# Kernel optimization log

Hardware: AMD Instinct MI355X
Metric: run time of the kernel (lower is better)

## Reference

```python
import jax, jax.numpy as jnp
import numpy as np

CH = 512
HEADS = 8
REDUCTION = 2
INNER = max(CH // REDUCTION, HEADS)  # 256
POS_RES = 16
LN_EPS = 1e-5


def setup_inputs() -> dict:
    key = jax.random.key(0)
    ks = jax.random.split(key, 7)
    B, H, W = 1, 64, 64
    x = jax.random.normal(ks[0], (B, CH, H, W), dtype=jnp.float32)
    w_qkv = jax.random.normal(ks[1], (INNER * 3, CH), dtype=jnp.float32) * 0.02
    w_proj = jax.random.normal(ks[2], (CH, INNER), dtype=jnp.float32) * 0.02
    b_proj = jnp.zeros((CH,), dtype=jnp.float32)
    pos_bias = jax.random.normal(ks[3], (1, HEADS, POS_RES, POS_RES), dtype=jnp.float32) * 0.02
    gamma = jnp.ones((CH,), dtype=jnp.float32)
    beta = jnp.zeros((CH,), dtype=jnp.float32)
    return {"x": x, "w_qkv": w_qkv, "w_proj": w_proj, "b_proj": b_proj,
            "pos_bias": pos_bias, "gamma": gamma, "beta": beta}


def reference(x, w_qkv, w_proj, b_proj, pos_bias, gamma, beta):
    B, C, H, W = x.shape
    d_head = INNER // HEADS
    scale = jnp.float32(d_head ** -0.5)

    # 1x1 conv == channel matmul
    qkv = jnp.einsum('oc,bchw->bohw', w_qkv, x)  # [B, 3*inner, H, W]
    q, k, v = jnp.split(qkv, 3, axis=1)

    def heads_view(t):
        return t.reshape(B, HEADS, d_head, H * W)  # [B, h, d, HW]

    q, k, v = heads_view(q), heads_view(k), heads_view(v)

    attn = jnp.einsum('bhdi,bhdj->bhij', q * scale, k)  # [B, h, HW, HW]

    # bilinear interp of pos bias 16x16 -> HxW (half-pixel, matches align_corners=False)
    pos = jax.image.resize(pos_bias, (1, HEADS, H, W), method='bilinear')
    pos = pos.reshape(1, HEADS, H * W)
    attn = attn + pos[..., :, None] + pos[..., None, :]

    attn = jax.nn.softmax(attn, axis=-1)
    y = jnp.einsum('bhij,bhdj->bhdi', attn, v)  # [B, h, d, HW]
    y = y.reshape(B, INNER, H, W)

    y = jnp.einsum('co,bohw->bchw', w_proj, y) + b_proj[None, :, None, None]

    # LayerNorm over channel dim of (x + y)
    z = (x + y).transpose(0, 2, 3, 1)  # [B, H, W, C]
    mu = jnp.mean(z, axis=-1, keepdims=True)
    var = jnp.var(z, axis=-1, keepdims=True)
    z = (z - mu) / jnp.sqrt(var + LN_EPS) * gamma + beta
    return z.transpose(0, 3, 1, 2)
```

## Files before the change

### kernel.cpp

```cpp
#include <hip/hip_runtime.h>
#include <hip/hip_bf16.h>
#include <math.h>

#define HW 4096
#define LN_EPS 1e-5f

typedef _Float16 half4v __attribute__((ext_vector_type(4)));
typedef _Float16 half8v __attribute__((ext_vector_type(8)));
typedef float float4v __attribute__((ext_vector_type(4)));
typedef __fp16 fp16v2 __attribute__((ext_vector_type(2)));
typedef __fp16 fp16v4 __attribute__((ext_vector_type(4)));

#if __has_builtin(__builtin_amdgcn_exp2f)
#define EXP2F(x) __builtin_amdgcn_exp2f(x)
#else
#define EXP2F(x) exp2f(x)
#endif

__device__ __forceinline__ half4v lo4(half8v v) { return __builtin_shufflevector(v, v, 0, 1, 2, 3); }
__device__ __forceinline__ half4v hi4(half8v v) { return __builtin_shufflevector(v, v, 4, 5, 6, 7); }

__device__ __forceinline__ void gload_lds16(const _Float16* g, _Float16* l) {
#if __has_builtin(__builtin_amdgcn_global_load_lds)
    __builtin_amdgcn_global_load_lds(
        (const __attribute__((address_space(1))) void*)(const void*)g,
        (__attribute__((address_space(3))) void*)(void*)l, 16, 0, 0);
#else
    int lane = threadIdx.x & 63;
    *(half8v*)(l + lane * 8) = *(const half8v*)g;
#endif
}

__global__ __launch_bounds__(256) void k_pre(const float* __restrict__ x,
                                             const float* __restrict__ wq,
                                             const float* __restrict__ wp,
                                             const float* __restrict__ pb,
                                             _Float16* __restrict__ xt,
                                             _Float16* __restrict__ wqh,
                                             _Float16* __restrict__ wph,
                                             float* __restrict__ pos) {
    int bx = blockIdx.x, t = threadIdx.x;
    if (bx < 512) {
        __shared__ _Float16 tile[64][65];
        int c0 = (bx >> 6) * 64, p0 = (bx & 63) * 64;
        int w = t >> 6, lane = t & 63;
        #pragma unroll
        for (int r = 0; r < 16; r++)
            tile[w * 16 + r][lane] = (_Float16)x[(c0 + w * 16 + r) * HW + p0 + lane];
        __syncthreads();
        int cg = (t & 15) * 4, pr = t >> 4;
        #pragma unroll
        for (int r = 0; r < 4; r++) {
            int p = pr + r * 16;
            half4v v;
            #pragma unroll
            for (int k = 0; k < 4; k++) v[k] = tile[cg + k][p];
            *(half4v*)&xt[(p0 + p) * 512 + c0 + cg] = v;
        }
        return;
    }
    int i = (bx - 512) * 256 + t;
    const float qs = 0.17677669529663687f * 1.4426950408889634f;
    if (i < 49152) {
        float s = (i < 16384) ? qs : 1.0f;
        float4v a = *(const float4v*)(wq + i * 8);
        float4v b = *(const float4v*)(wq + i * 8 + 4);
        half8v h;
        #pragma unroll
        for (int k = 0; k < 4; k++) { h[k] = (_Float16)(a[k] * s); h[4 + k] = (_Float16)(b[k] * s); }
        *(half8v*)(wqh + i * 8) = h;
    } else if (i < 65536) {
        int j = i - 49152;
        float4v a = *(const float4v*)(wp + j * 8);
        float4v b = *(const float4v*)(wp + j * 8 + 4);
        half8v h;
        #pragma unroll
        for (int k = 0; k < 4; k++) { h[k] = (_Float16)a[k]; h[4 + k] = (_Float16)b[k]; }
        *(half8v*)(wph + j * 8) = h;
    } else {
        int j = i - 65536;
        int h = j >> 12, p = j & 4095, y = p >> 6, xx = p & 63;
        float sy = y * 0.25f - 0.375f, sx = xx * 0.25f - 0.375f;
        float fy = floorf(sy), fx = floorf(sx);
        float wy = sy - fy, wx = sx - fx;
        int y0 = (int)fy, x0 = (int)fx;
        int y1 = y0 + 1 < 15 ? y0 + 1 : 15;
        int x1 = x0 + 1 < 15 ? x0 + 1 : 15;
        y0 = y0 > 0 ? y0 : 0;
        x0 = x0 > 0 ? x0 : 0;
        const float* src = pb + h * 256;
        float v = (1.f - wy) * ((1.f - wx) * src[y0 * 16 + x0] + wx * src[y0 * 16 + x1]) +
                  wy * ((1.f - wx) * src[y1 * 16 + x0] + wx * src[y1 * 16 + x1]);
        pos[j] = v * 1.4426950408889634f;
    }
}

__global__ __launch_bounds__(256) void k_qkv(const _Float16* __restrict__ wqh,
                                             const _Float16* __restrict__ xt,
                                             _Float16* __restrict__ qa,
                                             _Float16* __restrict__ ka,
                                             _Float16* __restrict__ va) {
    int n0 = (blockIdx.x >> 5) * 64;
    int p0 = (blockIdx.x & 31) * 128;
    int t = threadIdx.x, w = t >> 6, lane = t & 63, quad = lane >> 4, l16 = lane & 15;

    const _Float16* aptr0 = xt + (p0 + w * 16 + l16) * 512 + quad * 8;
    const _Float16* aptr1 = aptr0 + 64 * 512;
    const _Float16* bptr = wqh + (n0 + l16) * 512 + quad * 8;

    float4v acc[2][4] = {};
    #pragma unroll 4
    for (int kc = 0; kc < 16; kc++) {
        half8v a0 = *(const half8v*)(aptr0 + kc * 32);
        half8v a1 = *(const half8v*)(aptr1 + kc * 32);
        #pragma unroll
        for (int nt = 0; nt < 4; nt++) {
            half8v b = *(const half8v*)(bptr + nt * 16 * 512 + kc * 32);
            acc[0][nt] = __builtin_amdgcn_mfma_f32_16x16x32_f16(a0, b, acc[0][nt], 0, 0, 0);
            acc[1][nt] = __builtin_amdgcn_mfma_f32_16x16x32_f16(a1, b, acc[1][nt], 0, 0, 0);
        }
    }
    #pragma unroll
    for (int ps = 0; ps < 2; ps++) {
        #pragma unroll
        for (int nt = 0; nt < 4; nt++) {
            int o = n0 + nt * 16 + l16;
            #pragma unroll
            for (int r = 0; r < 4; r++) {
                int p = p0 + ps * 64 + w * 16 + quad * 4 + r;
                _Float16 v = (_Float16)acc[ps][nt][r];
                if (o < 256) {
                    qa[(o >> 5) * 131072 + p * 32 + (o & 31)] = v;
                } else if (o < 512) {
                    int oc = o - 256, hh = oc >> 5, d = oc & 31;
                    ka[hh * 131072 + (p >> 4) * 512 + ((d >> 3) * 16 + (p & 15)) * 8 + (d & 7)] = v;
                } else {
                    int oc = o - 512, hh = oc >> 5, d = oc & 31;
                    va[hh * 131072 + (p >> 4) * 512 + (((p >> 2) & 3) * 16 + (d & 15)) * 8 +
                       (d >> 4) * 4 + (p & 3)] = v;
                }
            }
        }
    }
}

__global__ __launch_bounds__(256, 4) void k_attn(const _Float16* __restrict__ qa,
                                                 const _Float16* __restrict__ ka,
                                                 const _Float16* __restrict__ va,
                                                 const float* __restrict__ pos,
                                                 float* __restrict__ op,
                                                 float* __restrict__ lp) {
    __shared__ __attribute__((aligned(16))) _Float16 kbuf[2][2048];
    __shared__ __attribute__((aligned(16))) _Float16 vbuf[2][2048];
    __shared__ __attribute__((aligned(16))) float posl[1024];
    int h = blockIdx.x & 7;
    int jq = (blockIdx.x >> 3) & 3;
    int qb = blockIdx.x >> 5;
    int t = threadIdx.x, w = t >> 6, lane = t & 63, quad = lane >> 4, l16 = lane & 15;
    int q0 = qb * 128 + w * 32;

    float* opp = op + jq * 1048576;
    float* lpp = lp + jq * 32768;

    *(float4v*)(posl + t * 4) = *(const float4v*)(pos + h * HW + jq * 1024 + t * 4);

    half8v qf0 = *(const half8v*)(qa + h * 131072 + (q0 + l16) * 32 + quad * 8);
    half8v qf1 = *(const half8v*)(qa + h * 131072 + (q0 + 16 + l16) * 32 + quad * 8);

    const _Float16* kg = ka + h * 131072 + jq * 32768;
    const _Float16* vg = va + h * 131072 + jq * 32768;

    gload_lds16(kg + (w * 64 + lane) * 8, &kbuf[0][w * 512]);
    gload_lds16(vg + (w * 64 + lane) * 8, &vbuf[0][w * 512]);

    float4v o00 = {}, o01 = {}, o10 = {}, o11 = {};
    float lsum0 = 0.f, lsum1 = 0.f;
    const fp16v2 one2 = {(__fp16)1.0f, (__fp16)1.0f};

    for (int tile = 0; tile < 16; tile++) {
        int buf = tile & 1;
        __syncthreads();
        if (tile + 1 < 16) {
            gload_lds16(kg + (tile + 1) * 2048 + (w * 64 + lane) * 8, &kbuf[buf ^ 1][w * 512]);
            gload_lds16(vg + (tile + 1) * 2048 + (w * 64 + lane) * 8, &vbuf[buf ^ 1][w * 512]);
        }
        #pragma unroll
        for (int w16 = 0; w16 < 4; w16++) {
            half8v kf = *(const half8v*)(kbuf[buf] + w16 * 512 + lane * 8);
            half8v vf = *(const half8v*)(vbuf[buf] + w16 * 512 + lane * 8);
            float4v pbv = *(const float4v*)(posl + tile * 64 + w16 * 16 + quad * 4);

            float4v s0 = __builtin_amdgcn_mfma_f32_16x16x32_f16(kf, qf0, pbv, 0, 0, 0);
            float4v s1 = __builtin_amdgcn_mfma_f32_16x16x32_f16(kf, qf1, pbv, 0, 0, 0);

            float e0 = EXP2F(s0[0]);
            float e1 = EXP2F(s0[1]);
            float e2 = EXP2F(s0[2]);
            float e3 = EXP2F(s0[3]);
            float f0 = EXP2F(s1[0]);
            float f1 = EXP2F(s1[1]);
            float f2 = EXP2F(s1[2]);
            float f3 = EXP2F(s1[3]);

            fp16v2 a01 = __builtin_amdgcn_cvt_pkrtz(e0, e1);
            fp16v2 a23 = __builtin_amdgcn_cvt_pkrtz(e2, e3);
            fp16v2 b01 = __builtin_amdgcn_cvt_pkrtz(f0, f1);
            fp16v2 b23 = __builtin_amdgcn_cvt_pkrtz(f2, f3);
            half4v pa0 = __builtin_bit_cast(half4v, __builtin_shufflevector(a01, a23, 0, 1, 2, 3));
            half4v pa1 = __builtin_bit_cast(half4v, __builtin_shufflevector(b01, b23, 0, 1, 2, 3));

#if __has_builtin(__builtin_amdgcn_fdot2)
            lsum0 = __builtin_amdgcn_fdot2(a01, one2, lsum0, false);
            lsum0 = __builtin_amdgcn_fdot2(a23, one2, lsum0, false);
            lsum1 = __builtin_amdgcn_fdot2(b01, one2, lsum1, false);
            lsum1 = __builtin_amdgcn_fdot2(b23, one2, lsum1, false);
#else
            lsum0 += (e0 + e1) + (e2 + e3);
            lsum1 += (f0 + f1) + (f2 + f3);
#endif
            o00 = __builtin_amdgcn_mfma_f32_16x16x16f16(pa0, lo4(vf), o00, 0, 0, 0);
            o01 = __builtin_amdgcn_mfma_f32_16x16x16f16(pa0, hi4(vf), o01, 0, 0, 0);
            o10 = __builtin_amdgcn_mfma_f32_16x16x16f16(pa1, lo4(vf), o10, 0, 0, 0);
            o11 = __builtin_amdgcn_mfma_f32_16x16x16f16(pa1, hi4(vf), o11, 0, 0, 0);
        }
    }
    lsum0 += __shfl_xor(lsum0, 16, 64);
    lsum0 += __shfl_xor(lsum0, 32, 64);
    lsum1 += __shfl_xor(lsum1, 16, 64);
    lsum1 += __shfl_xor(lsum1, 32, 64);
    #pragma unroll
    for (int r = 0; r < 4; r++) {
        int qr = quad * 4 + r;
        int qi0 = q0 + qr, qi1 = q0 + 16 + qr;
        opp[qi0 * 256 + h * 32 + l16] = o00[r];
        opp[qi0 * 256 + h * 32 + 16 + l16] = o01[r];
        opp[qi1 * 256 + h * 32 + l16] = o10[r];
        opp[qi1 * 256 + h * 32 + 16 + l16] = o11[r];
    }
    if (quad == 0) {
        lpp[(q0 + l16) * 8 + h] = lsum0;
        lpp[(q0 + 16 + l16) * 8 + h] = lsum1;
    }
}

__global__ __launch_bounds__(1024) void k_proj_ln(const _Float16* __restrict__ wph,
                                                  const float* __restrict__ op,
                                                  const float* __restrict__ lp,
                                                  const float* __restrict__ x,
                                                  const float* __restrict__ b_proj,
                                                  const float* __restrict__ gamma,
                                                  const float* __restrict__ beta,
                                                  float* __restrict__ out) {
    __shared__ __attribute__((aligned(16))) _Float16 ys[16 * 264];
    __shared__ float red[2][16][17];
    int p0 = blockIdx.x * 16;
    int t = threadIdx.x, w = t >> 6, lane = t & 63, quad = lane >> 4, l16 = lane & 15;
    {
        int p = t >> 6, cg = (t & 63) * 4;
        int pi = p0 + p;
        float4v a0 = *(const float4v*)(op + pi * 256 + cg);
        float4v a1 = *(const float4v*)(op + 1048576 + pi * 256 + cg);
        float4v a2 = *(const float4v*)(op + 2097152 + pi * 256 + cg);
        float4v a3 = *(const float4v*)(op + 3145728 + pi * 256 + cg);
        int hh = cg >> 5;
        float l = lp[pi * 8 + hh] + lp[32768 + pi * 8 + hh] +
                  lp[65536 + pi * 8 + hh] + lp[98304 + pi * 8 + hh];
        float inv = 1.f / l;
        half4v y;
        #pragma unroll
        for (int k = 0; k < 4; k++) y[k] = (_Float16)(((a0[k] + a1[k]) + (a2[k] + a3[k])) * inv);
        *(half4v*)(ys + p * 264 + cg) = y;
    }
    __syncthreads();
    float4v acc[2] = {};
    #pragma unroll
    for (int kc = 0; kc < 8; kc++) {
        half8v b = *(const half8v*)(ys + l16 * 264 + kc * 32 + quad * 8);
        #pragma unroll
        for (int mt = 0; mt < 2; mt++) {
            half8v a = *(const half8v*)(wph + (w * 32 + mt * 16 + l16) * 256 + kc * 32 + quad * 8);
            acc[mt] = __builtin_amdgcn_mfma_f32_16x16x32_f16(a, b, acc[mt], 0, 0, 0);
        }
    }
    int p = p0 + l16;
    float sum = 0.f, sumsq = 0.f;
    #pragma unroll
    for (int mt = 0; mt < 2; mt++)
        #pragma unroll
        for (int r = 0; r < 4; r++) {
            int c = w * 32 + mt * 16 + quad * 4 + r;
            float v = acc[mt][r] + b_proj[c] + x[c * HW + p];
            acc[mt][r] = v;
            sum += v;
            sumsq += v * v;
        }
    sum += __shfl_xor(sum, 16, 64);
    sum += __shfl_xor(sum, 32, 64);
    sumsq += __shfl_xor(sumsq, 16, 64);
    sumsq += __shfl_xor(sumsq, 32, 64);
    if (quad == 0) { red[0][w][l16] = sum; red[1][w][l16] = sumsq; }
    __syncthreads();
    float s0 = 0.f, s1 = 0.f;
    #pragma unroll
    for (int ww = 0; ww < 16; ww++) { s0 += red[0][ww][l16]; s1 += red[1][ww][l16]; }
    float mean = s0 * (1.f / 512.f);
    float var = s1 * (1.f / 512.f) - mean * mean;
    float rstd = rsqrtf(var + LN_EPS);
    #pragma unroll
    for (int mt = 0; mt < 2; mt++)
        #pragma unroll
        for (int r = 0; r < 4; r++) {
            int c = w * 32 + mt * 16 + quad * 4 + r;
            out[c * HW + p] = (acc[mt][r] - mean) * rstd * gamma[c] + beta[c];
        }
}

extern "C" void kernel_launch(void* const* d_in, const int* in_sizes, int n_in,
                              void* d_out, int out_size, void* d_ws, size_t ws_size,
                              hipStream_t stream) {
    const float* x      = (const float*)d_in[0];
    const float* w_qkv  = (const float*)d_in[1];
    const float* w_proj = (const float*)d_in[2];
    const float* b_proj = (const float*)d_in[3];
    const float* pos_b  = (const float*)d_in[4];
    const float* gamma  = (const float*)d_in[5];
    const float* beta   = (const float*)d_in[6];
    char* ws = (char*)d_ws;
    _Float16* xt  = (_Float16*)(ws);
    _Float16* qa  = (_Float16*)(ws + 4194304);
    _Float16* ka  = (_Float16*)(ws + 6291456);
    _Float16* va  = (_Float16*)(ws + 8388608);
    float*    op  = (float*)   (ws + 10485760);
    float*    lp  = (float*)   (ws + 27262976);
    float*    pos = (float*)   (ws + 27787264);
    _Float16* wqh = (_Float16*)(ws + 27918336);
    _Float16* wph = (_Float16*)(ws + 28704768);

    k_pre<<<896, 256, 0, stream>>>(x, w_qkv, w_proj, pos_b, xt, wqh, wph, pos);
    k_qkv<<<384, 256, 0, stream>>>(wqh, xt, qa, ka, va);
    k_attn<<<1024, 256, 0, stream>>>(qa, ka, va, pos, op, lp);
    k_proj_ln<<<256, 1024, 0, stream>>>(wph, op, lp, x, b_proj, gamma, beta, (float*)d_out);
}
```

Before: 139.9 us.

## Fuse four stages into one cooperative persistent kernel with grid syncs

Merges the preprocessing, QKV projection, attention and projection+LayerNorm stages into a single cooperative kernel that separates phases with grid-wide barriers. The goal is to remove the overhead and tail gaps of four separate kernel launches. To keep one 256-thread block shape across all phases, the QKV GEMM tile is halved and the proj/LN phase moves from 1024 to 256 threads, each wave covering 128 channels. This costs more per-thread register pressure in the LN phase, grid-sync overhead, and possible occupancy limits on the fused kernel. Separate kernels remain as a fallback if the cooperative launch fails.

```diff
diff --git a/kernel.cpp b/kernel.cpp
--- a/kernel.cpp
+++ b/kernel.cpp
@@ -1,15 +1,17 @@
 #include <hip/hip_runtime.h>
 #include <hip/hip_bf16.h>
+#include <hip/hip_cooperative_groups.h>
 #include <math.h>
 
 #define HW 4096
 #define LN_EPS 1e-5f
+
+namespace cg = cooperative_groups;
 
 typedef _Float16 half4v __attribute__((ext_vector_type(4)));
 typedef _Float16 half8v __attribute__((ext_vector_type(8)));
 typedef float float4v __attribute__((ext_vector_type(4)));
 typedef __fp16 fp16v2 __attribute__((ext_vector_type(2)));
-typedef __fp16 fp16v4 __attribute__((ext_vector_type(4)));
 
 #if __has_builtin(__builtin_amdgcn_exp2f)
 #define EXP2F(x) __builtin_amdgcn_exp2f(x)
@@ -31,52 +33,52 @@
 #endif
 }
 
-__global__ __launch_bounds__(256) void k_pre(const float* __restrict__ x,
-                                             const float* __restrict__ wq,
-                                             const float* __restrict__ wp,
-                                             const float* __restrict__ pb,
-                                             _Float16* __restrict__ xt,
-                                             _Float16* __restrict__ wqh,
-                                             _Float16* __restrict__ wph,
-                                             float* __restrict__ pos) {
-    int bx = blockIdx.x, t = threadIdx.x;
-    if (bx < 512) {
-        __shared__ _Float16 tile[64][65];
-        int c0 = (bx >> 6) * 64, p0 = (bx & 63) * 64;
-        int w = t >> 6, lane = t & 63;
+struct P {
+    const float *x, *wq, *wp, *b_proj, *pb, *gamma, *beta;
+    _Float16 *xt, *qa, *ka, *va;
+    float *op, *lp, *pos;
+    _Float16 *wqh, *wph;
+    float* out;
+};
+
+__device__ __forceinline__ void phaseA(int u, int t, char* smem, const P& pp) {
+    int w = t >> 6, lane = t & 63;
+    if (u < 512) {
+        _Float16 (*tile)[65] = (_Float16(*)[65])smem;
+        int c0 = (u >> 6) * 64, p0 = (u & 63) * 64;
         #pragma unroll
         for (int r = 0; r < 16; r++)
-            tile[w * 16 + r][lane] = (_Float16)x[(c0 + w * 16 + r) * HW + p0 + lane];
+            tile[w * 16 + r][lane] = (_Float16)pp.x[(c0 + w * 16 + r) * HW + p0 + lane];
         __syncthreads();
-        int cg = (t & 15) * 4, pr = t >> 4;
+        int cgx = (t & 15) * 4, pr = t >> 4;
         #pragma unroll
         for (int r = 0; r < 4; r++) {
             int p = pr + r * 16;
             half4v v;
             #pragma unroll
-            for (int k = 0; k < 4; k++) v[k] = tile[cg + k][p];
-            *(half4v*)&xt[(p0 + p) * 512 + c0 + cg] = v;
+            for (int k = 0; k < 4; k++) v[k] = tile[cgx + k][p];
+            *(half4v*)&pp.xt[(p0 + p) * 512 + c0 + cgx] = v;
         }
         return;
     }
-    int i = (bx - 512) * 256 + t;
+    int i = (u - 512) * 256 + t;
     const float qs = 0.17677669529663687f * 1.4426950408889634f;
     if (i < 49152) {
         float s = (i < 16384) ? qs : 1.0f;
-        float4v a = *(const float4v*)(wq + i * 8);
-        float4v b = *(const float4v*)(wq + i * 8 + 4);
+        float4v a = *(const float4v*)(pp.wq + i * 8);
+        float4v b = *(const float4v*)(pp.wq + i * 8 + 4);
         half8v h;
         #pragma unroll
         for (int k = 0; k < 4; k++) { h[k] = (_Float16)(a[k] * s); h[4 + k] = (_Float16)(b[k] * s); }
-        *(half8v*)(wqh + i * 8) = h;
+        *(half8v*)(pp.wqh + i * 8) = h;
     } else if (i < 65536) {
         int j = i - 49152;
-        float4v a = *(const float4v*)(wp + j * 8);
-        float4v b = *(const float4v*)(wp + j * 8 + 4);
+        float4v a = *(const float4v*)(pp.wp + j * 8);
+        float4v b = *(const float4v*)(pp.wp + j * 8 + 4);
         half8v h;
         #pragma unroll
         for (int k = 0; k < 4; k++) { h[k] = (_Float16)a[k]; h[4 + k] = (_Float16)b[k]; }
-        *(half8v*)(wph + j * 8) = h;
+        *(half8v*)(pp.wph + j * 8) = h;
     } else {
         int j = i - 65536;
         int h = j >> 12, p = j & 4095, y = p >> 6, xx = p & 63;
@@ -88,90 +90,72 @@
         int x1 = x0 + 1 < 15 ? x0 + 1 : 15;
         y0 = y0 > 0 ? y0 : 0;
         x0 = x0 > 0 ? x0 : 0;
-        const float* src = pb + h * 256;
+        const float* src = pp.pb + h * 256;
         float v = (1.f - wy) * ((1.f - wx) * src[y0 * 16 + x0] + wx * src[y0 * 16 + x1]) +
                   wy * ((1.f - wx) * src[y1 * 16 + x0] + wx * src[y1 * 16 + x1]);
-        pos[j] = v * 1.4426950408889634f;
-    }
-}
-
-__global__ __launch_bounds__(256) void k_qkv(const _Float16* __restrict__ wqh,
-                                             const _Float16* __restrict__ xt,
-                                             _Float16* __restrict__ qa,
-                                             _Float16* __restrict__ ka,
-                                             _Float16* __restrict__ va) {
-    int n0 = (blockIdx.x >> 5) * 64;
-    int p0 = (blockIdx.x & 31) * 128;
-    int t = threadIdx.x, w = t >> 6, lane = t & 63, quad = lane >> 4, l16 = lane & 15;
-
-    const _Float16* aptr0 = xt + (p0 + w * 16 + l16) * 512 + quad * 8;
-    const _Float16* aptr1 = aptr0 + 64 * 512;
-    const _Float16* bptr = wqh + (n0 + l16) * 512 + quad * 8;
-
-    float4v acc[2][4] = {};
+        pp.pos[j] = v * 1.4426950408889634f;
+    }
+}
+
+__device__ __forceinline__ void phaseB(int u, int t, const P& pp) {
+    int w = t >> 6, lane = t & 63, quad = lane >> 4, l16 = lane & 15;
+    int n0 = (u >> 6) * 64;
+    int p0 = (u & 63) * 64;
+    const _Float16* aptr = pp.xt + (p0 + w * 16 + l16) * 512 + quad * 8;
+    const _Float16* bptr = pp.wqh + (n0 + l16) * 512 + quad * 8;
+    float4v acc[4] = {};
     #pragma unroll 4
     for (int kc = 0; kc < 16; kc++) {
-        half8v a0 = *(const half8v*)(aptr0 + kc * 32);
-        half8v a1 = *(const half8v*)(aptr1 + kc * 32);
+        half8v a = *(const half8v*)(aptr + kc * 32);
         #pragma unroll
         for (int nt = 0; nt < 4; nt++) {
             half8v b = *(const half8v*)(bptr + nt * 16 * 512 + kc * 32);
-            acc[0][nt] = __builtin_amdgcn_mfma_f32_16x16x32_f16(a0, b, acc[0][nt], 0, 0, 0);
-            acc[1][nt] = __builtin_amdgcn_mfma_f32_16x16x32_f16(a1, b, acc[1][nt], 0, 0, 0);
-        }
-    }
-    #pragma unroll
-    for (int ps = 0; ps < 2; ps++) {
-        #pragma unroll
-        for (int nt = 0; nt < 4; nt++) {
-            int o = n0 + nt * 16 + l16;
-            #pragma unroll
-            for (int r = 0; r < 4; r++) {
-                int p = p0 + ps * 64 + w * 16 + quad * 4 + r;
-                _Float16 v = (_Float16)acc[ps][nt][r];
-                if (o < 256) {
-                    qa[(o >> 5) * 131072 + p * 32 + (o & 31)] = v;
-                } else if (o < 512) {
-                    int oc = o - 256, hh = oc >> 5, d = oc & 31;
-                    ka[hh * 131072 + (p >> 4) * 512 + ((d >> 3) * 16 + (p & 15)) * 8 + (d & 7)] = v;
-                } else {
-                    int oc = o - 512, hh = oc >> 5, d = oc & 31;
-                    va[hh * 131072 + (p >> 4) * 512 + (((p >> 2) & 3) * 16 + (d & 15)) * 8 +
-                       (d >> 4) * 4 + (p & 3)] = v;
-                }
+            acc[nt] = __builtin_amdgcn_mfma_f32_16x16x32_f16(a, b, acc[nt], 0, 0, 0);
+        }
+    }
+    #pragma unroll
+    for (int nt = 0; nt < 4; nt++) {
+        int o = n0 + nt * 16 + l16;
+        #pragma unroll
+        for (int r = 0; r < 4; r++) {
+            int p = p0 + w * 16 + quad * 4 + r;
+            _Float16 v = (_Float16)acc[nt][r];
+            if (o < 256) {
+                pp.qa[(o >> 5) * 131072 + p * 32 + (o & 31)] = v;
+            } else if (o < 512) {
+                int oc = o - 256, hh = oc >> 5, d = oc & 31;
+                pp.ka[hh * 131072 + (p >> 4) * 512 + ((d >> 3) * 16 + (p & 15)) * 8 + (d & 7)] = v;
+            } else {
+                int oc = o - 512, hh = oc >> 5, d = oc & 31;
+                pp.va[hh * 131072 + (p >> 4) * 512 + (((p >> 2) & 3) * 16 + (d & 15)) * 8 +
+                      (d >> 4) * 4 + (p & 3)] = v;
             }
         }
     }
 }
 
-__global__ __launch_bounds__(256, 4) void k_attn(const _Float16* __restrict__ qa,
-                                                 const _Float16* __restrict__ ka,
-                                                 const _Float16* __restrict__ va,
-                                                 const float* __restrict__ pos,
-                                                 float* __restrict__ op,
-                                                 float* __restrict__ lp) {
-    __shared__ __attribute__((aligned(16))) _Float16 kbuf[2][2048];
-    __shared__ __attribute__((aligned(16))) _Float16 vbuf[2][2048];
-    __shared__ __attribute__((aligned(16))) float posl[1024];
-    int h = blockIdx.x & 7;
-    int jq = (blockIdx.x >> 3) & 3;
-    int qb = blockIdx.x >> 5;
-    int t = threadIdx.x, w = t >> 6, lane = t & 63, quad = lane >> 4, l16 = lane & 15;
+__device__ __forceinline__ void phaseC(int u, int t, char* smem, const P& pp) {
+    _Float16* kbuf = (_Float16*)smem;
+    _Float16* vbuf = (_Float16*)(smem + 8192);
+    float* posl = (float*)(smem + 16384);
+    int w = t >> 6, lane = t & 63, quad = lane >> 4, l16 = lane & 15;
+    int h = u & 7;
+    int jq = (u >> 3) & 3;
+    int qb = u >> 5;
     int q0 = qb * 128 + w * 32;
-
-    float* opp = op + jq * 1048576;
-    float* lpp = lp + jq * 32768;
-
-    *(float4v*)(posl + t * 4) = *(const float4v*)(pos + h * HW + jq * 1024 + t * 4);
-
-    half8v qf0 = *(const half8v*)(qa + h * 131072 + (q0 + l16) * 32 + quad * 8);
-    half8v qf1 = *(const half8v*)(qa + h * 131072 + (q0 + 16 + l16) * 32 + quad * 8);
-
-    const _Float16* kg = ka + h * 131072 + jq * 32768;
-    const _Float16* vg = va + h * 131072 + jq * 32768;
-
-    gload_lds16(kg + (w * 64 + lane) * 8, &kbuf[0][w * 512]);
-    gload_lds16(vg + (w * 64 + lane) * 8, &vbuf[0][w * 512]);
+    float* opp = pp.op + jq * 1048576;
+    float* lpp = pp.lp + jq * 32768;
+
+    *(float4v*)(posl + t * 4) = *(const float4v*)(pp.pos + h * HW + jq * 1024 + t * 4);
+
+    half8v qf0 = *(const half8v*)(pp.qa + h * 131072 + (q0 + l16) * 32 + quad * 8);
+    half8v qf1 = *(const half8v*)(pp.qa + h * 131072 + (q0 + 16 + l16) * 32 + quad * 8);
+
+    const _Float16* kg = pp.ka + h * 131072 + jq * 32768;
+    const _Float16* vg = pp.va + h * 131072 + jq * 32768;
+
+    gload_lds16(kg + (w * 64 + lane) * 8, kbuf + w * 512);
+    gload_lds16(vg + (w * 64 + lane) * 8, vbuf + w * 512);
 
     float4v o00 = {}, o01 = {}, o10 = {}, o11 = {};
     float lsum0 = 0.f, lsum1 = 0.f;
@@ -181,13 +165,15 @@
         int buf = tile & 1;
         __syncthreads();
         if (tile + 1 < 16) {
-            gload_lds16(kg + (tile + 1) * 2048 + (w * 64 + lane) * 8, &kbuf[buf ^ 1][w * 512]);
-            gload_lds16(vg + (tile + 1) * 2048 + (w * 64 + lane) * 8, &vbuf[buf ^ 1][w * 512]);
+            gload_lds16(kg + (tile + 1) * 2048 + (w * 64 + lane) * 8,
+                        kbuf + (buf ^ 1) * 2048 + w * 512);
+            gload_lds16(vg + (tile + 1) * 2048 + (w * 64 + lane) * 8,
+                        vbuf + (buf ^ 1) * 2048 + w * 512);
         }
         #pragma unroll
         for (int w16 = 0; w16 < 4; w16++) {
-            half8v kf = *(const half8v*)(kbuf[buf] + w16 * 512 + lane * 8);
-            half8v vf = *(const half8v*)(vbuf[buf] + w16 * 512 + lane * 8);
+            half8v kf = *(const half8v*)(kbuf + buf * 2048 + w16 * 512 + lane * 8);
+            half8v vf = *(const half8v*)(vbuf + buf * 2048 + w16 * 512 + lane * 8);
             float4v pbv = *(const float4v*)(posl + tile * 64 + w16 * 16 + quad * 4);
 
             float4v s0 = __builtin_amdgcn_mfma_f32_16x16x32_f16(kf, qf0, pbv, 0, 0, 0);
@@ -243,53 +229,48 @@
     }
 }
 
-__global__ __launch_bounds__(1024) void k_proj_ln(const _Float16* __restrict__ wph,
-                                                  const float* __restrict__ op,
-                                                  const float* __restrict__ lp,
-                                                  const float* __restrict__ x,
-                                                  const float* __restrict__ b_proj,
-                                                  const float* __restrict__ gamma,
-                                                  const float* __restrict__ beta,
-                                                  float* __restrict__ out) {
-    __shared__ __attribute__((aligned(16))) _Float16 ys[16 * 264];
-    __shared__ float red[2][16][17];
-    int p0 = blockIdx.x * 16;
-    int t = threadIdx.x, w = t >> 6, lane = t & 63, quad = lane >> 4, l16 = lane & 15;
-    {
-        int p = t >> 6, cg = (t & 63) * 4;
+__device__ __forceinline__ void phaseD(int u, int t, char* smem, const P& pp) {
+    _Float16* ys = (_Float16*)smem;
+    float (*red)[4][16] = (float(*)[4][16])(smem + 8448);
+    int w = t >> 6, lane = t & 63, quad = lane >> 4, l16 = lane & 15;
+    int p0 = u * 16;
+    #pragma unroll
+    for (int g4 = 0; g4 < 4; g4++) {
+        int g = t + g4 * 256;
+        int p = g >> 6, cgx = (g & 63) * 4;
         int pi = p0 + p;
-        float4v a0 = *(const float4v*)(op + pi * 256 + cg);
-        float4v a1 = *(const float4v*)(op + 1048576 + pi * 256 + cg);
-        float4v a2 = *(const float4v*)(op + 2097152 + pi * 256 + cg);
-        float4v a3 = *(const float4v*)(op + 3145728 + pi * 256 + cg);
-        int hh = cg >> 5;
-        float l = lp[pi * 8 + hh] + lp[32768 + pi * 8 + hh] +
-                  lp[65536 + pi * 8 + hh] + lp[98304 + pi * 8 + hh];
+        float4v a0 = *(const float4v*)(pp.op + pi * 256 + cgx);
+        float4v a1 = *(const float4v*)(pp.op + 1048576 + pi * 256 + cgx);
+        float4v a2 = *(const float4v*)(pp.op + 2097152 + pi * 256 + cgx);
+        float4v a3 = *(const float4v*)(pp.op + 3145728 + pi * 256 + cgx);
+        int hh = cgx >> 5;
+        float l = pp.lp[pi * 8 + hh] + pp.lp[32768 + pi * 8 + hh] +
+                  pp.lp[65536 + pi * 8 + hh] + pp.lp[98304 + pi * 8 + hh];
         float inv = 1.f / l;
-        half4v y;
-        #pragma unroll
-        for (int k = 0; k < 4; k++) y[k] = (_Float16)(((a0[k] + a1[k]) + (a2[k] + a3[k])) * inv);
-        *(half4v*)(ys + p * 264 + cg) = y;
+        half4v yv;
+        #pragma unroll
+        for (int k = 0; k < 4; k++) yv[k] = (_Float16)(((a0[k] + a1[k]) + (a2[k] + a3[k])) * inv);
+        *(half4v*)(ys + p * 264 + cgx) = yv;
     }
     __syncthreads();
-    float4v acc[2] = {};
+    float4v acc[8] = {};
     #pragma unroll
     for (int kc = 0; kc < 8; kc++) {
         half8v b = *(const half8v*)(ys + l16 * 264 + kc * 32 + quad * 8);
         #pragma unroll
-        for (int mt = 0; mt < 2; mt++) {
-            half8v a = *(const half8v*)(wph + (w * 32 + mt * 16 + l16) * 256 + kc * 32 + quad * 8);
+        for (int mt = 0; mt < 8; mt++) {
+            half8v a = *(const half8v*)(pp.wph + (w * 128 + mt * 16 + l16) * 256 + kc * 32 + quad * 8);
             acc[mt] = __builtin_amdgcn_mfma_f32_16x16x32_f16(a, b, acc[mt], 0, 0, 0);
         }
     }
     int p = p0 + l16;
     float sum = 0.f, sumsq = 0.f;
     #pragma unroll
-    for (int mt = 0; mt < 2; mt++)
+    for (int mt = 0; mt < 8; mt++)
         #pragma unroll
         for (int r = 0; r < 4; r++) {
-            int c = w * 32 + mt * 16 + quad * 4 + r;
-            float v = acc[mt][r] + b_proj[c] + x[c * HW + p];
+            int c = w * 128 + mt * 16 + quad * 4 + r;
+            float v = acc[mt][r] + pp.b_proj[c] + pp.x[c * HW + p];
             acc[mt][r] = v;
             sum += v;
             sumsq += v * v;
@@ -300,44 +281,88 @@
     sumsq += __shfl_xor(sumsq, 32, 64);
     if (quad == 0) { red[0][w][l16] = sum; red[1][w][l16] = sumsq; }
     __syncthreads();
-    float s0 = 0.f, s1 = 0.f;
-    #pragma unroll
-    for (int ww = 0; ww < 16; ww++) { s0 += red[0][ww][l16]; s1 += red[1][ww][l16]; }
+    float s0 = (red[0][0][l16] + red[0][1][l16]) + (red[0][2][l16] + red[0][3][l16]);
+    float s1 = (red[1][0][l16] + red[1][1][l16]) + (red[1][2][l16] + red[1][3][l16]);
     float mean = s0 * (1.f / 512.f);
     float var = s1 * (1.f / 512.f) - mean * mean;
     float rstd = rsqrtf(var + LN_EPS);
     #pragma unroll
-    for (int mt = 0; mt < 2; mt++)
+    for (int mt = 0; mt < 8; mt++)
         #pragma unroll
         for (int r = 0; r < 4; r++) {
-            int c = w * 32 + mt * 16 + quad * 4 + r;
-            out[c * HW + p] = (acc[mt][r] - mean) * rstd * gamma[c] + beta[c];
-        }
+            int c = w * 128 + mt * 16 + quad * 4 + r;
+            pp.out[c * HW + p] = (acc[mt][r] - mean) * rstd * pp.gamma[c] + pp.beta[c];
+        }
+}
+
+__global__ __launch_bounds__(256, 4) void k_coop(P pp) {
+    __shared__ __attribute__((aligned(16))) char smem[24576];
+    cg::grid_group grid = cg::this_grid();
+    int G = gridDim.x, bid = blockIdx.x, t = threadIdx.x;
+    for (int u = bid; u < 896; u += G) { __syncthreads(); phaseA(u, t, smem, pp); }
+    __threadfence();
+    grid.sync();
+    for (int u = bid; u < 768; u += G) phaseB(u, t, pp);
+    __threadfence();
+    grid.sync();
+    for (int u = bid; u < 1024; u += G) { __syncthreads(); phaseC(u, t, smem, pp); }
+    __threadfence();
+    grid.sync();
+    for (int u = bid; u < 256; u += G) { __syncthreads(); phaseD(u, t, smem, pp); }
+}
+
+__global__ __launch_bounds__(256) void kA(P pp) {
+    __shared__ __attribute__((aligned(16))) char smem[8320];
+    phaseA(blockIdx.x, threadIdx.x, smem, pp);
+}
+__global__ __launch_bounds__(256) void kB(P pp) { phaseB(blockIdx.x, threadIdx.x, pp); }
+__global__ __launch_bounds__(256, 4) void kC(P pp) {
+    __shared__ __attribute__((aligned(16))) char smem[24576];
+    phaseC(blockIdx.x, threadIdx.x, smem, pp);
+}
+__global__ __launch_bounds__(256) void kD(P pp) {
+    __shared__ __attribute__((aligned(16))) char smem[9216];
+    phaseD(blockIdx.x, threadIdx.x, smem, pp);
 }
 
 extern "C" void kernel_launch(void* const* d_in, const int* in_sizes, int n_in,
                               void* d_out, int out_size, void* d_ws, size_t ws_size,
                               hipStream_t stream) {
-    const float* x      = (const float*)d_in[0];
-    const float* w_qkv  = (const float*)d_in[1];
-    const float* w_proj = (const float*)d_in[2];
-    const float* b_proj = (const float*)d_in[3];
-    const float* pos_b  = (const float*)d_in[4];
-    const float* gamma  = (const float*)d_in[5];
-    const float* beta   = (const float*)d_in[6];
     char* ws = (char*)d_ws;
-    _Float16* xt  = (_Float16*)(ws);
-    _Float16* qa  = (_Float16*)(ws + 4194304);
-    _Float16* ka  = (_Float16*)(ws + 6291456);
-    _Float16* va  = (_Float16*)(ws + 8388608);
-    float*    op  = (float*)   (ws + 10485760);
-    float*    lp  = (float*)   (ws + 27262976);
-    float*    pos = (float*)   (ws + 27787264);
-    _Float16* wqh = (_Float16*)(ws + 27918336);
-    _Float16* wph = (_Float16*)(ws + 28704768);
-
-    k_pre<<<896, 256, 0, stream>>>(x, w_qkv, w_proj, pos_b, xt, wqh, wph, pos);
-    k_qkv<<<384, 256, 0, stream>>>(wqh, xt, qa, ka, va);
-    k_attn<<<1024, 256, 0, stream>>>(qa, ka, va, pos, op, lp);
-    k_proj_ln<<<256, 1024, 0, stream>>>(wph, op, lp, x, b_proj, gamma, beta, (float*)d_out);
-}
+    P pp;
+    pp.x      = (const float*)d_in[0];
+    pp.wq     = (const float*)d_in[1];
+    pp.wp     = (const float*)d_in[2];
+    pp.b_proj = (const float*)d_in[3];
+    pp.pb     = (const float*)d_in[4];
+    pp.gamma  = (const float*)d_in[5];
+    pp.beta   = (const float*)d_in[6];
+    pp.xt  = (_Float16*)(ws);
+    pp.qa  = (_Float16*)(ws + 4194304);
+    pp.ka  = (_Float16*)(ws + 6291456);
+    pp.va  = (_Float16*)(ws + 8388608);
+    pp.op  = (float*)   (ws + 10485760);
+    pp.lp  = (float*)   (ws + 27262976);
+    pp.pos = (float*)   (ws + 27787264);
+    pp.wqh = (_Float16*)(ws + 27918336);
+    pp.wph = (_Float16*)(ws + 28704768);
+    pp.out = (float*)d_out;
+
+    int occ = 0;
+    hipError_t e = hipOccupancyMaxActiveBlocksPerMultiprocessor(&occ, (const void*)k_coop, 256, 0);
+    bool done = false;
+    if (e == hipSuccess && occ > 0) {
+        int grid = occ * 256;
+        if (grid > 1024) grid = 1024;
+        void* args[] = {&pp};
+        if (hipLaunchCooperativeKernel((void*)k_coop, dim3(grid), dim3(256), args, 0, stream)
+            == hipSuccess)
+            done = true;
+    }
+    if (!done) {
+        kA<<<896, 256, 0, stream>>>(pp);
+        kB<<<768, 256, 0, stream>>>(pp);
+        kC<<<1024, 256, 0, stream>>>(pp);
+        kD<<<256, 256, 0, stream>>>(pp);
+    }
+}
```

Result: slower. 537.1 us (+284.0%).

## Fuse preprocessing into QKV and attention kernels, drop pre-pass launch

Applied to the files above, without the earlier changes.

Removes the separate k_pre kernel. The QKV GEMM now reads fp32 x directly, transposes and converts it through an LDS tile, and converts and scales w_qkv on the fly. The proj-weight conversion moves into the first 128 QKV blocks, and the bilinear pos-bias interpolation is computed per attention block in shared memory. This saves a launch and the xt/pos intermediate round-trips through HBM, at the cost of redundant weight conversion across blocks, strided uncoalesced-ish fp32 loads of x, and extra per-block setup work in attention.

```diff
diff --git a/kernel.cpp b/kernel.cpp
--- a/kernel.cpp
+++ b/kernel.cpp
@@ -9,7 +9,6 @@
 typedef _Float16 half8v __attribute__((ext_vector_type(8)));
 typedef float float4v __attribute__((ext_vector_type(4)));
 typedef __fp16 fp16v2 __attribute__((ext_vector_type(2)));
-typedef __fp16 fp16v4 __attribute__((ext_vector_type(4)));
 
 #if __has_builtin(__builtin_amdgcn_exp2f)
 #define EXP2F(x) __builtin_amdgcn_exp2f(x)
@@ -31,93 +30,63 @@
 #endif
 }
 
-__global__ __launch_bounds__(256) void k_pre(const float* __restrict__ x,
+__global__ __launch_bounds__(256) void k_qkv(const float* __restrict__ x,
                                              const float* __restrict__ wq,
                                              const float* __restrict__ wp,
-                                             const float* __restrict__ pb,
-                                             _Float16* __restrict__ xt,
-                                             _Float16* __restrict__ wqh,
                                              _Float16* __restrict__ wph,
-                                             float* __restrict__ pos) {
-    int bx = blockIdx.x, t = threadIdx.x;
-    if (bx < 512) {
-        __shared__ _Float16 tile[64][65];
-        int c0 = (bx >> 6) * 64, p0 = (bx & 63) * 64;
-        int w = t >> 6, lane = t & 63;
-        #pragma unroll
-        for (int r = 0; r < 16; r++)
-            tile[w * 16 + r][lane] = (_Float16)x[(c0 + w * 16 + r) * HW + p0 + lane];
-        __syncthreads();
-        int cg = (t & 15) * 4, pr = t >> 4;
-        #pragma unroll
-        for (int r = 0; r < 4; r++) {
-            int p = pr + r * 16;
-            half4v v;
-            #pragma unroll
-            for (int k = 0; k < 4; k++) v[k] = tile[cg + k][p];
-            *(half4v*)&xt[(p0 + p) * 512 + c0 + cg] = v;
-        }
-        return;
-    }
-    int i = (bx - 512) * 256 + t;
-    const float qs = 0.17677669529663687f * 1.4426950408889634f;
-    if (i < 49152) {
-        float s = (i < 16384) ? qs : 1.0f;
-        float4v a = *(const float4v*)(wq + i * 8);
-        float4v b = *(const float4v*)(wq + i * 8 + 4);
-        half8v h;
-        #pragma unroll
-        for (int k = 0; k < 4; k++) { h[k] = (_Float16)(a[k] * s); h[4 + k] = (_Float16)(b[k] * s); }
-        *(half8v*)(wqh + i * 8) = h;
-    } else if (i < 65536) {
-        int j = i - 49152;
-        float4v a = *(const float4v*)(wp + j * 8);
-        float4v b = *(const float4v*)(wp + j * 8 + 4);
-        half8v h;
-        #pragma unroll
-        for (int k = 0; k < 4; k++) { h[k] = (_Float16)a[k]; h[4 + k] = (_Float16)b[k]; }
-        *(half8v*)(wph + j * 8) = h;
-    } else {
-        int j = i - 65536;
-        int h = j >> 12, p = j & 4095, y = p >> 6, xx = p & 63;
-        float sy = y * 0.25f - 0.375f, sx = xx * 0.25f - 0.375f;
-        float fy = floorf(sy), fx = floorf(sx);
-        float wy = sy - fy, wx = sx - fx;
-        int y0 = (int)fy, x0 = (int)fx;
-        int y1 = y0 + 1 < 15 ? y0 + 1 : 15;
-        int x1 = x0 + 1 < 15 ? x0 + 1 : 15;
-        y0 = y0 > 0 ? y0 : 0;
-        x0 = x0 > 0 ? x0 : 0;
-        const float* src = pb + h * 256;
-        float v = (1.f - wy) * ((1.f - wx) * src[y0 * 16 + x0] + wx * src[y0 * 16 + x1]) +
-                  wy * ((1.f - wx) * src[y1 * 16 + x0] + wx * src[y1 * 16 + x1]);
-        pos[j] = v * 1.4426950408889634f;
-    }
-}
-
-__global__ __launch_bounds__(256) void k_qkv(const _Float16* __restrict__ wqh,
-                                             const _Float16* __restrict__ xt,
                                              _Float16* __restrict__ qa,
                                              _Float16* __restrict__ ka,
                                              _Float16* __restrict__ va) {
-    int n0 = (blockIdx.x >> 5) * 64;
-    int p0 = (blockIdx.x & 31) * 128;
-    int t = threadIdx.x, w = t >> 6, lane = t & 63, quad = lane >> 4, l16 = lane & 15;
-
-    const _Float16* aptr0 = xt + (p0 + w * 16 + l16) * 512 + quad * 8;
-    const _Float16* aptr1 = aptr0 + 64 * 512;
-    const _Float16* bptr = wqh + (n0 + l16) * 512 + quad * 8;
+    __shared__ __attribute__((aligned(16))) _Float16 xs[128][72];
+    int bid = blockIdx.x, t = threadIdx.x;
+    int w = t >> 6, lane = t & 63, quad = lane >> 4, l16 = lane & 15;
+    const float qs = 0.17677669529663687f * 1.4426950408889634f;
+
+    if (bid < 128) {
+        int i = bid * 1024 + t * 4;
+        float4v a = *(const float4v*)(wp + i);
+        half4v h;
+        #pragma unroll
+        for (int k = 0; k < 4; k++) h[k] = (_Float16)a[k];
+        *(half4v*)(wph + i) = h;
+    }
+
+    int n0 = (bid >> 5) * 64;
+    int p0 = (bid & 31) * 128;
+    int sp = t & 127;
+    int sg = (t >> 7) * 32;
 
     float4v acc[2][4] = {};
-    #pragma unroll 4
-    for (int kc = 0; kc < 16; kc++) {
-        half8v a0 = *(const half8v*)(aptr0 + kc * 32);
-        half8v a1 = *(const half8v*)(aptr1 + kc * 32);
-        #pragma unroll
-        for (int nt = 0; nt < 4; nt++) {
-            half8v b = *(const half8v*)(bptr + nt * 16 * 512 + kc * 32);
-            acc[0][nt] = __builtin_amdgcn_mfma_f32_16x16x32_f16(a0, b, acc[0][nt], 0, 0, 0);
-            acc[1][nt] = __builtin_amdgcn_mfma_f32_16x16x32_f16(a1, b, acc[1][nt], 0, 0, 0);
+    for (int k0 = 0; k0 < 512; k0 += 64) {
+        __syncthreads();
+        #pragma unroll
+        for (int cc8 = 0; cc8 < 4; cc8++) {
+            int cb = sg + cc8 * 8;
+            half8v v;
+            #pragma unroll
+            for (int c = 0; c < 8; c++) v[c] = (_Float16)x[(k0 + cb + c) * HW + p0 + sp];
+            *(half8v*)&xs[sp][cb] = v;
+        }
+        __syncthreads();
+        #pragma unroll
+        for (int kc2 = 0; kc2 < 2; kc2++) {
+            half8v a0 = *(const half8v*)&xs[w * 16 + l16][kc2 * 32 + quad * 8];
+            half8v a1 = *(const half8v*)&xs[64 + w * 16 + l16][kc2 * 32 + quad * 8];
+            #pragma unroll
+            for (int nt = 0; nt < 4; nt++) {
+                float s = (n0 + nt * 16 < 256) ? qs : 1.0f;
+                const float* wr = wq + (n0 + nt * 16 + l16) * 512 + k0 + kc2 * 32 + quad * 8;
+                float4v b0 = *(const float4v*)wr;
+                float4v b1 = *(const float4v*)(wr + 4);
+                half8v b;
+                #pragma unroll
+                for (int k = 0; k < 4; k++) {
+                    b[k] = (_Float16)(b0[k] * s);
+                    b[4 + k] = (_Float16)(b1[k] * s);
+                }
+                acc[0][nt] = __builtin_amdgcn_mfma_f32_16x16x32_f16(a0, b, acc[0][nt], 0, 0, 0);
+                acc[1][nt] = __builtin_amdgcn_mfma_f32_16x16x32_f16(a1, b, acc[1][nt], 0, 0, 0);
+            }
         }
     }
     #pragma unroll
@@ -147,31 +116,49 @@
 __global__ __launch_bounds__(256, 4) void k_attn(const _Float16* __restrict__ qa,
                                                  const _Float16* __restrict__ ka,
                                                  const _Float16* __restrict__ va,
-                                                 const float* __restrict__ pos,
+                                                 const float* __restrict__ pb,
                                                  float* __restrict__ op,
                                                  float* __restrict__ lp) {
-    __shared__ __attribute__((aligned(16))) _Float16 kbuf[2][2048];
-    __shared__ __attribute__((aligned(16))) _Float16 vbuf[2][2048];
-    __shared__ __attribute__((aligned(16))) float posl[1024];
+    __shared__ __attribute__((aligned(16))) char smem[21504];
+    _Float16* kbuf = (_Float16*)smem;
+    _Float16* vbuf = (_Float16*)(smem + 8192);
+    float* posl = (float*)(smem + 16384);
+    float* pbl = (float*)(smem + 20480);
     int h = blockIdx.x & 7;
     int jq = (blockIdx.x >> 3) & 3;
     int qb = blockIdx.x >> 5;
     int t = threadIdx.x, w = t >> 6, lane = t & 63, quad = lane >> 4, l16 = lane & 15;
     int q0 = qb * 128 + w * 32;
-
     float* opp = op + jq * 1048576;
     float* lpp = lp + jq * 32768;
 
-    *(float4v*)(posl + t * 4) = *(const float4v*)(pos + h * HW + jq * 1024 + t * 4);
+    const _Float16* kg = ka + h * 131072 + jq * 32768;
+    const _Float16* vg = va + h * 131072 + jq * 32768;
+
+    gload_lds16(kg + (w * 64 + lane) * 8, kbuf + w * 512);
+    gload_lds16(vg + (w * 64 + lane) * 8, vbuf + w * 512);
+
+    pbl[t] = pb[h * 256 + t];
+    __syncthreads();
+    #pragma unroll
+    for (int k = 0; k < 4; k++) {
+        int j = jq * 1024 + t * 4 + k;
+        int y = j >> 6, xx = j & 63;
+        float sy = y * 0.25f - 0.375f, sx = xx * 0.25f - 0.375f;
+        float fy = floorf(sy), fx = floorf(sx);
+        float wy = sy - fy, wx = sx - fx;
+        int y0 = (int)fy, x0 = (int)fx;
+        int y1 = y0 + 1 < 15 ? y0 + 1 : 15;
+        int x1 = x0 + 1 < 15 ? x0 + 1 : 15;
+        y0 = y0 > 0 ? y0 : 0;
+        x0 = x0 > 0 ? x0 : 0;
+        float v = (1.f - wy) * ((1.f - wx) * pbl[y0 * 16 + x0] + wx * pbl[y0 * 16 + x1]) +
+                  wy * ((1.f - wx) * pbl[y1 * 16 + x0] + wx * pbl[y1 * 16 + x1]);
+        posl[t * 4 + k] = v * 1.4426950408889634f;
+    }
 
     half8v qf0 = *(const half8v*)(qa + h * 131072 + (q0 + l16) * 32 + quad * 8);
     half8v qf1 = *(const half8v*)(qa + h * 131072 + (q0 + 16 + l16) * 32 + quad * 8);
-
-    const _Float16* kg = ka + h * 131072 + jq * 32768;
-    const _Float16* vg = va + h * 131072 + jq * 32768;
-
-    gload_lds16(kg + (w * 64 + lane) * 8, &kbuf[0][w * 512]);
-    gload_lds16(vg + (w * 64 + lane) * 8, &vbuf[0][w * 512]);
 
     float4v o00 = {}, o01 = {}, o10 = {}, o11 = {};
     float lsum0 = 0.f, lsum1 = 0.f;
@@ -181,13 +168,15 @@
         int buf = tile & 1;
         __syncthreads();
         if (tile + 1 < 16) {
-            gload_lds16(kg + (tile + 1) * 2048 + (w * 64 + lane) * 8, &kbuf[buf ^ 1][w * 512]);
-            gload_lds16(vg + (tile + 1) * 2048 + (w * 64 + lane) * 8, &vbuf[buf ^ 1][w * 512]);
+            gload_lds16(kg + (tile + 1) * 2048 + (w * 64 + lane) * 8,
+                        kbuf + (buf ^ 1) * 2048 + w * 512);
+            gload_lds16(vg + (tile + 1) * 2048 + (w * 64 + lane) * 8,
+                        vbuf + (buf ^ 1) * 2048 + w * 512);
         }
         #pragma unroll
         for (int w16 = 0; w16 < 4; w16++) {
-            half8v kf = *(const half8v*)(kbuf[buf] + w16 * 512 + lane * 8);
-            half8v vf = *(const half8v*)(vbuf[buf] + w16 * 512 + lane * 8);
+            half8v kf = *(const half8v*)(kbuf + buf * 2048 + w16 * 512 + lane * 8);
+            half8v vf = *(const half8v*)(vbuf + buf * 2048 + w16 * 512 + lane * 8);
             float4v pbv = *(const float4v*)(posl + tile * 64 + w16 * 16 + quad * 4);
 
             float4v s0 = __builtin_amdgcn_mfma_f32_16x16x32_f16(kf, qf0, pbv, 0, 0, 0);
@@ -326,18 +315,14 @@
     const float* gamma  = (const float*)d_in[5];
     const float* beta   = (const float*)d_in[6];
     char* ws = (char*)d_ws;
-    _Float16* xt  = (_Float16*)(ws);
-    _Float16* qa  = (_Float16*)(ws + 4194304);
-    _Float16* ka  = (_Float16*)(ws + 6291456);
-    _Float16* va  = (_Float16*)(ws + 8388608);
-    float*    op  = (float*)   (ws + 10485760);
-    float*    lp  = (float*)   (ws + 27262976);
-    float*    pos = (float*)   (ws + 27787264);
-    _Float16* wqh = (_Float16*)(ws + 27918336);
-    _Float16* wph = (_Float16*)(ws + 28704768);
-
-    k_pre<<<896, 256, 0, stream>>>(x, w_qkv, w_proj, pos_b, xt, wqh, wph, pos);
-    k_qkv<<<384, 256, 0, stream>>>(wqh, xt, qa, ka, va);
-    k_attn<<<1024, 256, 0, stream>>>(qa, ka, va, pos, op, lp);
+    _Float16* qa  = (_Float16*)(ws);
+    _Float16* ka  = (_Float16*)(ws + 2097152);
+    _Float16* va  = (_Float16*)(ws + 4194304);
+    float*    op  = (float*)   (ws + 6291456);
+    float*    lp  = (float*)   (ws + 23068672);
+    _Float16* wph = (_Float16*)(ws + 23592960);
+
+    k_qkv<<<384, 256, 0, stream>>>(x, w_qkv, w_proj, wph, qa, ka, va);
+    k_attn<<<1024, 256, 0, stream>>>(qa, ka, va, pos_b, op, lp);
     k_proj_ln<<<256, 1024, 0, stream>>>(wph, op, lp, x, b_proj, gamma, beta, (float*)d_out);
 }
```

After: 152.1 us. +8.8%, slower.
